# Optimization experiments

Measured on AMD Instinct MI355X. Metric: run time of the kernel, lower is better.

## Reference

```python
import jax, jax.numpy as jnp
import numpy as np

B, T, C = 1, 2048, 1024
H, HKV, DH, WIN = 16, 4, 64, 128
EPS = 1e-5


def rotate_half(x):
    x1, x2 = jnp.split(x, 2, axis=-1)
    return jnp.concatenate((-x2, x1), axis=-1)


def setup_inputs() -> dict:
    key = jax.random.key(0)
    ks = jax.random.split(key, 8)
    s = 0.02
    return {
        "x": jax.random.normal(ks[0], (B, T, C), dtype=jnp.float32),
        "Wq": jax.random.normal(ks[1], (C, H * DH), dtype=jnp.float32) * s,
        "Wk": jax.random.normal(ks[2], (C, HKV * DH), dtype=jnp.float32) * s,
        "Wv": jax.random.normal(ks[3], (C, HKV * DH), dtype=jnp.float32) * s,
        "Wc": jax.random.normal(ks[4], (C, C), dtype=jnp.float32) * s,
        "Wg": jax.random.normal(ks[5], (C, H), dtype=jnp.float32) * s,
        "bg": jax.random.normal(ks[6], (H,), dtype=jnp.float32) * s,
        "rms_w": jnp.ones((C,), dtype=jnp.float32),
    }


def reference(x, Wq, Wk, Wv, Wc, Wg, bg, rms_w):
    n_rep = H // HKV
    # projections -> [B, heads, T, DH]
    q = (x @ Wq).reshape(B, T, H, DH).transpose(0, 2, 1, 3)
    k = (x @ Wk).reshape(B, T, HKV, DH).transpose(0, 2, 1, 3)
    v = (x @ Wv).reshape(B, T, HKV, DH).transpose(0, 2, 1, 3)
    # rotary embedding (freqs duplicated across the two halves)
    inv_freq = 1.0 / (10000.0 ** (jnp.arange(0, DH, 2, dtype=jnp.float32) / DH))
    freqs = jnp.arange(T, dtype=jnp.float32)[:, None] * inv_freq[None, :]
    emb = jnp.concatenate((freqs, freqs), axis=-1)  # [T, DH]
    cos, sin = jnp.cos(emb)[None, None], jnp.sin(emb)[None, None]
    q = q * cos + rotate_half(q) * sin
    k = k * cos + rotate_half(k) * sin
    # GQA: repeat kv heads (contiguous repeat matches torch expand+reshape)
    k = jnp.repeat(k, n_rep, axis=1)
    v = jnp.repeat(v, n_rep, axis=1)
    # gated decay
    gate_logits = (x @ Wg + bg).reshape(B, T, H, 1).transpose(0, 2, 1, 3)  # [B,H,T,1]
    log_alpha = jax.nn.log_sigmoid(gate_logits)
    log_in_scale = jax.nn.log_sigmoid(-gate_logits)
    k_scaled = k * jnp.exp(log_in_scale)
    la_cum = jnp.cumsum(log_alpha, axis=2)                  # [B,H,T,1]
    log_decay = la_cum - jnp.swapaxes(la_cum, 2, 3)         # [B,H,T,T]
    causal = jnp.triu(jnp.ones((T, T), dtype=bool), k=1)
    decay = jnp.exp(jnp.where(causal, -jnp.inf, log_decay))
    scores = jnp.einsum('bhtd,bhsd->bhts', q, k_scaled)
    y_global = jnp.einsum('bhts,bhsd->bhtd', scores * decay, v)
    nb = T // WIN
    qb = q.reshape(B, H, nb, WIN, DH)
    kb = k.reshape(B, H, nb, WIN, DH)
    vb = v.reshape(B, H, nb, WIN, DH)
    att = jnp.einsum('bhnqd,bhnkd->bhnqk', qb, kb) / jnp.sqrt(jnp.float32(DH))
    wmask = jnp.triu(jnp.ones((WIN, WIN), dtype=bool), k=1)
    att = jax.nn.softmax(jnp.where(wmask, -jnp.inf, att), axis=-1)
    y_local = jnp.einsum('bhnqk,bhnkd->bhnqd', att, vb).reshape(B, H, T, DH)
    # fuse, RMSNorm, output projection
    y = (y_global + y_local).transpose(0, 2, 1, 3).reshape(B, T, C)
    y = y * jax.lax.rsqrt(jnp.mean(y * y, axis=-1, keepdims=True) + EPS) * rms_w
    return y @ Wc
```

## Files before the change

### kernel.cpp

```cpp
#include <hip/hip_runtime.h>
#include <hip/hip_bf16.h>


typedef __attribute__((ext_vector_type(8))) short bf16x8;
typedef __attribute__((ext_vector_type(4))) float f32x4;

#define MFMA16(a, b, c) __builtin_amdgcn_mfma_f32_16x16x32_bf16(a, b, c, 0, 0, 0)
#define LN10000_OVER_32 0.28782313662425575f

__device__ __forceinline__ short f2b(float f) {
  __hip_bfloat16 h = __float2bfloat16(f);
  return *reinterpret_cast<short*>(&h);
}
__device__ __forceinline__ float b2f(short s) {
  return __uint_as_float(((unsigned)(unsigned short)s) << 16);
}
__device__ __forceinline__ void gload16(const void* g, void* l) {
  __builtin_amdgcn_global_load_lds(
      (const __attribute__((address_space(1))) void*)g,
      (__attribute__((address_space(3))) void*)l, 16, 0, 0);
}

__device__ __forceinline__ void transpose_cvt64(
    const float* __restrict__ src, short* __restrict__ dst, int R, int C,
    int bx, int by, float* ts , const float* __restrict__ sw) {
  int c0 = bx * 64, r0 = by * 64;
  int tr = threadIdx.x >> 4, tc4 = (threadIdx.x & 15) * 4;
#pragma unroll
  for (int p = 0; p < 4; ++p) {
    int row = p * 16 + tr;
    float4 v = *(const float4*)&src[(size_t)(r0 + row) * C + c0 + tc4];
    ts[row * 65 + tc4] = v.x;
    ts[row * 65 + tc4 + 1] = v.y;
    ts[row * 65 + tc4 + 2] = v.z;
    ts[row * 65 + tc4 + 3] = v.w;
  }
  __syncthreads();
#pragma unroll
  for (int p = 0; p < 4; ++p) {
    int cr = p * 16 + tr;
    alignas(8) short o[4];
#pragma unroll
    for (int i = 0; i < 4; ++i) {
      int rr = tc4 + i;
      float m = sw ? sw[r0 + rr] : 1.0f;
      o[i] = f2b(ts[rr * 65 + cr] * m);
    }
    *(uint2*)&dst[(size_t)(c0 + cr) * R + r0 + tc4] = *(uint2*)o;
  }
}

__global__ __launch_bounds__(256) void prep_fused(
    const float* __restrict__ x, const float* __restrict__ Wq,
    const float* __restrict__ Wk, const float* __restrict__ Wv,
    const float* __restrict__ Wc, const float* __restrict__ Wg,
    const float* __restrict__ bg, const float* __restrict__ rmsw,
    short* __restrict__ xb, short* __restrict__ wqkvT,
    short* __restrict__ wcT, float* __restrict__ g, float* __restrict__ rs) {
  __shared__ float sbuf[64 * 65];
  const int j = blockIdx.x;
  const int tid = threadIdx.x;
  if (j < 1024) {
    const int i = j * 2048 + tid * 8;
    float4 a = *(const float4*)(x + i);
    float4 b = *(const float4*)(x + i + 4);
    alignas(16) short o[8] = {f2b(a.x), f2b(a.y), f2b(a.z), f2b(a.w),
                              f2b(b.x), f2b(b.y), f2b(b.z), f2b(b.w)};
    *(float4*)(xb + i) = *(float4*)o;
    float* xs = sbuf;
    float* part = sbuf + 2048;
    *(float4*)(xs + tid * 8) = a;
    *(float4*)(xs + tid * 8 + 4) = b;
    __syncthreads();
    const int h = tid & 15, ch = (tid >> 4) & 7, row = tid >> 7;
    const float* xr = xs + row * 1024 + ch * 128;
    const float* wgp = Wg + (size_t)(ch * 128) * 16 + h;
    float acc = 0.f;
#pragma unroll 8
    for (int k = 0; k < 128; ++k) acc = fmaf(xr[k], wgp[k * 16], acc);
    part[row * 128 + ch * 16 + h] = acc;
    __syncthreads();
    if (tid < 32) {
      int rr = tid >> 4, hh = tid & 15;
      float s = bg[hh];
#pragma unroll
      for (int cc = 0; cc < 8; ++cc) s += part[rr * 128 + cc * 16 + hh];
      g[(j * 2 + rr) * 16 + hh] = s;
    }
  } else if (j < 1280) {
    int jj = j - 1024;
    transpose_cvt64(Wq, wqkvT, 1024, 1024, jj & 15, jj >> 4, sbuf, nullptr);
  } else if (j < 1344) {
    int jj = j - 1280;
    transpose_cvt64(Wk, wqkvT + 1024 * 1024, 1024, 256, jj & 3, jj >> 2, sbuf,
                    nullptr);
  } else if (j < 1408) {
    int jj = j - 1344;
    transpose_cvt64(Wv, wqkvT + 1280 * 1024, 1024, 256, jj & 3, jj >> 2, sbuf,
                    nullptr);
  } else if (j < 1664) {
    int jj = j - 1408;
    transpose_cvt64(Wc, wcT, 1024, 1024, jj & 15, jj >> 4, sbuf, rmsw);
  } else {
    int i4 = ((j - 1664) * 256 + tid) * 4;
    float4 z = {0.f, 0.f, 0.f, 0.f};
    *(float4*)(rs + i4) = z;
  }
}

__global__ __launch_bounds__(256) void qkv_gemm_fused(
    const short* __restrict__ A, const short* __restrict__ Bt,
    short* __restrict__ qkvb, short* __restrict__ vtb,
    short* __restrict__ ktb, const float* __restrict__ g,
    float* __restrict__ lac, float* __restrict__ insc) {
  __shared__ short As[128 * 64];
  __shared__ short Bs[64 * 64];
  __shared__ float part[256];
  const int id = blockIdx.x;
  const int tid = threadIdx.x;
  if (id >= 384) {
    const int h = id - 384;
    float vals[8];
    float local = 0.f;
#pragma unroll
    for (int i = 0; i < 8; ++i) {
      int t = tid * 8 + i;
      float gv = g[t * 16 + h];
      float la = (gv > 0.f) ? -log1pf(expf(-gv)) : (gv - log1pf(expf(gv)));
      insc[h * 2048 + t] = 1.f / (1.f + expf(gv));
      vals[i] = la;
      local += la;
    }
    part[tid] = local;
    __syncthreads();
    for (int off = 1; off < 256; off <<= 1) {
      float add = (tid >= off) ? part[tid - off] : 0.f;
      __syncthreads();
      part[tid] += add;
      __syncthreads();
    }
    float run = (tid > 0) ? part[tid - 1] : 0.f;
#pragma unroll
    for (int i = 0; i < 8; ++i) {
      run += vals[i];
      lac[h * 2048 + tid * 8 + i] = run;
    }
    return;
  }
  const int lane = tid & 63, wid = tid >> 6;
  const int l15 = lane & 15, lq = lane >> 4;
  const int jlin = id >> 3;
  const int by = (id & 7) + 8 * (jlin / 24);
  const int bx = jlin % 24;
  const int m0 = by * 128, n0 = bx * 64;
  const int K = 1024;
  const int srow = lane >> 3;
  const int sc16 = (lane & 7) ^ srow;
  f32x4 acc[2][4];
#pragma unroll
  for (int mt = 0; mt < 2; ++mt)
#pragma unroll
    for (int nt = 0; nt < 4; ++nt) acc[mt][nt] = {0.f, 0.f, 0.f, 0.f};
  for (int kt = 0; kt < K; kt += 64) {
    __syncthreads();
#pragma unroll
    for (int i = 0; i < 4; ++i) {
      int jj = wid * 4 + i;
      int row = jj * 8 + srow;
      gload16(A + (size_t)(m0 + row) * K + kt + sc16 * 8, &As[jj * 512]);
    }
#pragma unroll
    for (int i = 0; i < 2; ++i) {
      int jj = wid * 2 + i;
      int row = jj * 8 + srow;
      gload16(Bt + (size_t)(n0 + row) * K + kt + sc16 * 8, &Bs[jj * 512]);
    }
    __syncthreads();
    bf16x8 af[2][2], bfr[4][2];
#pragma unroll
    for (int ks = 0; ks < 2; ++ks) {
      int c16 = ks * 4 + lq;
#pragma unroll
      for (int mt = 0; mt < 2; ++mt) {
        int ar = wid * 32 + mt * 16 + l15;
        af[mt][ks] = *(const bf16x8*)&As[(ar * 8 + (c16 ^ (ar & 7))) * 8];
      }
#pragma unroll
      for (int nt = 0; nt < 4; ++nt) {
        int br = nt * 16 + l15;
        bfr[nt][ks] = *(const bf16x8*)&Bs[(br * 8 + (c16 ^ (br & 7))) * 8];
      }
    }
#pragma unroll
    for (int ks = 0; ks < 2; ++ks)
#pragma unroll
      for (int mt = 0; mt < 2; ++mt)
#pragma unroll
        for (int nt = 0; nt < 4; ++nt)
          acc[mt][nt] = MFMA16(af[mt][ks], bfr[nt][ks], acc[mt][nt]);
  }
  if (bx >= 20) {
#pragma unroll
    for (int mt = 0; mt < 2; ++mt) {
      int row0 = m0 + wid * 32 + mt * 16 + lq * 4;
#pragma unroll
      for (int nt = 0; nt < 4; ++nt) {
        int vcol = (n0 - 1280) + nt * 16 + l15;
        alignas(8) short o4[4];
#pragma unroll
        for (int r = 0; r < 4; ++r) o4[r] = f2b(acc[mt][nt][r]);
        *(uint2*)&vtb[(size_t)vcol * 2048 + row0] = *(uint2*)o4;
      }
    }
    return;
  }
  const bool isk = (bx >= 16);
#pragma unroll
  for (int mt = 0; mt < 2; ++mt) {
    int row0 = m0 + wid * 32 + mt * 16 + lq * 4;
#pragma unroll
    for (int nt = 0; nt < 2; ++nt) {
      int d = nt * 16 + l15;
      float ivf = __expf(-LN10000_OVER_32 * (float)d);
      alignas(8) short oa[4], ob[4];
#pragma unroll
      for (int r = 0; r < 4; ++r) {
        int row_g = row0 + r;
        float th = (float)row_g * ivf;
        float cs = cosf(th), sn = sinf(th);
        float a = acc[mt][nt][r], b = acc[mt][nt + 2][r];
        oa[r] = f2b(a * cs - b * sn);
        ob[r] = f2b(b * cs + a * sn);
        qkvb[(size_t)row_g * 1536 + n0 + d] = oa[r];
        qkvb[(size_t)row_g * 1536 + n0 + d + 32] = ob[r];
      }
      if (isk) {
        int dk = n0 - 1024 + d;
        *(uint2*)&ktb[(size_t)dk * 2048 + row0] = *(uint2*)oa;
        *(uint2*)&ktb[(size_t)(dk + 32) * 2048 + row0] = *(uint2*)ob;
      }
    }
  }
}

__global__ __launch_bounds__(256) void chunk_state(
    const short* __restrict__ vtb, const short* __restrict__ ktb,
    const float* __restrict__ lac, const float* __restrict__ insc,
    short* __restrict__ Bmat) {
  __shared__ short Ks[64 * 64], Vts[64 * 64];
  __shared__ float lacs[64], inss[64], gvals[64];
  const int tid = threadIdx.x, lane = tid & 63, wid = tid >> 6;
  const int l15 = lane & 15, lq = lane >> 4;
  const int h = blockIdx.y, kh = h >> 2, c = blockIdx.x;
  const int srow = lane >> 3;
  const int sc16 = (lane & 7) ^ srow;
#pragma unroll
  for (int i = 0; i < 2; ++i) {
    int jj = wid * 2 + i;
    int row = jj * 8 + srow;
    gload16(ktb + (size_t)(kh * 64 + row) * 2048 + c * 64 + sc16 * 8,
            &Ks[jj * 512]);
    gload16(vtb + (size_t)(kh * 64 + row) * 2048 + c * 64 + sc16 * 8,
            &Vts[jj * 512]);
  }
  if (tid < 64) {
    lacs[tid] = lac[h * 2048 + c * 64 + tid];
    inss[tid] = insc[h * 2048 + c * 64 + tid];
  }
  __syncthreads();
  if (tid < 64)
    gvals[tid] = __expf(fminf(lacs[63] - lacs[tid], 0.f)) * inss[tid];
  __syncthreads();
  const int er = wid * 16 + l15;
  bf16x8 av[2];
#pragma unroll
  for (int ks = 0; ks < 2; ++ks) {
    int c16 = ks * 4 + lq;
    bf16x8 raw = *(const bf16x8*)&Vts[(er * 8 + (c16 ^ (er & 7))) * 8];
    float4 g0 = *(const float4*)&gvals[c16 * 8];
    float4 g1 = *(const float4*)&gvals[c16 * 8 + 4];
    float gv[8] = {g0.x, g0.y, g0.z, g0.w, g1.x, g1.y, g1.z, g1.w};
    bf16x8 sc;
#pragma unroll
    for (int jx = 0; jx < 8; ++jx) sc[jx] = f2b(b2f(raw[jx]) * gv[jx]);
    av[ks] = sc;
  }
  f32x4 acc[4];
#pragma unroll
  for (int nt = 0; nt < 4; ++nt) acc[nt] = {0.f, 0.f, 0.f, 0.f};
#pragma unroll
  for (int ks = 0; ks < 2; ++ks) {
    int c16 = ks * 4 + lq;
#pragma unroll
    for (int nt = 0; nt < 4; ++nt) {
      int dr = nt * 16 + l15;
      bf16x8 bk = *(const bf16x8*)&Ks[(dr * 8 + (c16 ^ (dr & 7))) * 8];
      acc[nt] = MFMA16(av[ks], bk, acc[nt]);
    }
  }
  short* Bout = Bmat + (size_t)(h * 32 + c) * 4096;
#pragma unroll
  for (int nt = 0; nt < 4; ++nt)
#pragma unroll
    for (int r = 0; r < 4; ++r) {
      int e = wid * 16 + lq * 4 + r;
      Bout[e * 64 + nt * 16 + l15] = f2b(acc[nt][r]);
    }
}

__global__ __launch_bounds__(256) void scan_kernel(
    const short* __restrict__ Bmat, const float* __restrict__ lac,
    short* __restrict__ St) {
  const int h = blockIdx.x, sl = blockIdx.y, tid = threadIdx.x;
  __shared__ float lacE[32];
  if (tid < 32) lacE[tid] = lac[h * 2048 + tid * 64 + 63];
  __syncthreads();
  const int base = sl * 512 + tid * 2;
  float S0 = 0.f, S1 = 0.f;
  *(unsigned*)&St[(size_t)(h * 32) * 4096 + base] = 0u;
  unsigned p = *(const unsigned*)&Bmat[(size_t)(h * 32) * 4096 + base];
  for (int c = 1; c < 32; ++c) {
    unsigned n = p;
    if (c < 31)
      n = *(const unsigned*)&Bmat[(size_t)(h * 32 + c) * 4096 + base];
    float a = (c >= 2) ? __expf(fminf(lacE[c - 1] - lacE[c - 2], 0.f)) : 0.f;
    S0 = fmaf(a, S0, b2f((short)(p & 0xffffu)));
    S1 = fmaf(a, S1, b2f((short)(p >> 16)));
    unsigned pack = (unsigned)(unsigned short)f2b(S0) |
                    ((unsigned)(unsigned short)f2b(S1) << 16);
    *(unsigned*)&St[(size_t)(h * 32 + c) * 4096 + base] = pack;
    p = n;
  }
}

__global__ __launch_bounds__(256) void fused_attn(
    const short* __restrict__ qkv, const short* __restrict__ vtb,
    const short* __restrict__ St, const float* __restrict__ lac,
    const float* __restrict__ insc, short* __restrict__ ys,
    float* __restrict__ rs) {
  const int c = blockIdx.x, h = blockIdx.y;
  const int kh = h >> 2;
  const bool odd = (c & 1) != 0;
  __shared__ short Qs[64 * 64], Kd[64 * 64], Vd[64 * 64], Sts[64 * 64],
      Kp[64 * 64], Vp[64 * 64], Pd[64 * 64], Pp[64 * 64];
  __shared__ float lacq[64], inss[64];
  __shared__ float laprev_sh;
  const int tid = threadIdx.x, lane = tid & 63, wid = tid >> 6;
  const int l15 = lane & 15, lq = lane >> 4;
  const int srow = lane >> 3;
  const int sc16 = (lane & 7) ^ srow;
#pragma unroll
  for (int i = 0; i < 2; ++i) {
    int jj = wid * 2 + i;
    int row = jj * 8 + srow;
    gload16(qkv + (size_t)(c * 64 + row) * 1536 + h * 64 + sc16 * 8,
            &Qs[jj * 512]);
    gload16(qkv + (size_t)(c * 64 + row) * 1536 + 1024 + kh * 64 + sc16 * 8,
            &Kd[jj * 512]);
    gload16(vtb + (size_t)(kh * 64 + row) * 2048 + c * 64 + sc16 * 8,
            &Vd[jj * 512]);
    gload16(St + (size_t)(h * 32 + c) * 4096 + row * 64 + sc16 * 8,
            &Sts[jj * 512]);
  }
  if (odd) {
#pragma unroll
    for (int i = 0; i < 2; ++i) {
      int jj = wid * 2 + i;
      int row = jj * 8 + srow;
      gload16(qkv + (size_t)((c - 1) * 64 + row) * 1536 + 1024 + kh * 64 +
                  sc16 * 8,
              &Kp[jj * 512]);
      gload16(vtb + (size_t)(kh * 64 + row) * 2048 + (c - 1) * 64 + sc16 * 8,
              &Vp[jj * 512]);
    }
  }
  if (tid < 64) {
    lacq[tid] = lac[h * 2048 + c * 64 + tid];
    inss[tid] = insc[h * 2048 + c * 64 + tid];
  }
  if (tid == 0) laprev_sh = (c > 0) ? lac[h * 2048 + c * 64 - 1] : 1e30f;
  __syncthreads();
  const int qr = wid * 16 + l15;
  bf16x8 aq[2];
#pragma unroll
  for (int ks = 0; ks < 2; ++ks) {
    int c16 = ks * 4 + lq;
    aq[ks] = *(const bf16x8*)&Qs[(qr * 8 + (c16 ^ (qr & 7))) * 8];
  }
  f32x4 sv[4];
#pragma unroll
  for (int nt = 0; nt < 4; ++nt) {
    int kr = nt * 16 + l15;
    bf16x8 bk0 = *(const bf16x8*)&Kd[(kr * 8 + ((0 + lq) ^ (kr & 7))) * 8];
    bf16x8 bk1 = *(const bf16x8*)&Kd[(kr * 8 + ((4 + lq) ^ (kr & 7))) * 8];
    f32x4 z = {0.f, 0.f, 0.f, 0.f};
    z = MFMA16(aq[0], bk0, z);
    z = MFMA16(aq[1], bk1, z);
    sv[nt] = z;
  }
  f32x4 sp[4];
  if (odd) {
#pragma unroll
    for (int nt = 0; nt < 4; ++nt) {
      int kr = nt * 16 + l15;
      bf16x8 bk0 = *(const bf16x8*)&Kp[(kr * 8 + ((0 + lq) ^ (kr & 7))) * 8];
      bf16x8 bk1 = *(const bf16x8*)&Kp[(kr * 8 + ((4 + lq) ^ (kr & 7))) * 8];
      f32x4 z = {0.f, 0.f, 0.f, 0.f};
      z = MFMA16(aq[0], bk0, z);
      z = MFMA16(aq[1], bk1, z);
      sp[nt] = z;
    }
  } else {
#pragma unroll
    for (int nt = 0; nt < 4; ++nt) sp[nt] = {0.f, 0.f, 0.f, 0.f};
  }
  f32x4 oi[4];
#pragma unroll
  for (int nt = 0; nt < 4; ++nt) {
    int er = nt * 16 + l15;
    bf16x8 bs0 = *(const bf16x8*)&Sts[(er * 8 + ((0 + lq) ^ (er & 7))) * 8];
    bf16x8 bs1 = *(const bf16x8*)&Sts[(er * 8 + ((4 + lq) ^ (er & 7))) * 8];
    f32x4 z = {0.f, 0.f, 0.f, 0.f};
    z = MFMA16(aq[0], bs0, z);
    z = MFMA16(aq[1], bs1, z);
    oi[nt] = z;
  }
  float mrow[4], ssum[4];
  float vd[4][4], vp[4][4];
#pragma unroll
  for (int r = 0; r < 4; ++r) mrow[r] = -1e30f;
#pragma unroll
  for (int nt = 0; nt < 4; ++nt) {
    int col = nt * 16 + l15;
#pragma unroll
    for (int r = 0; r < 4; ++r) {
      int row = wid * 16 + lq * 4 + r;
      float xv = (col <= row) ? sv[nt][r] * 0.125f : -1e30f;
      vd[nt][r] = xv;
      mrow[r] = fmaxf(mrow[r], xv);
      if (odd) {
        float xp = sp[nt][r] * 0.125f;
        vp[nt][r] = xp;
        mrow[r] = fmaxf(mrow[r], xp);
      }
    }
  }
#pragma unroll
  for (int r = 0; r < 4; ++r) {
    for (int off = 1; off < 16; off <<= 1)
      mrow[r] = fmaxf(mrow[r], __shfl_xor(mrow[r], off, 64));
    ssum[r] = 0.f;
  }
#pragma unroll
  for (int nt = 0; nt < 4; ++nt) {
#pragma unroll
    for (int r = 0; r < 4; ++r) {
      float e = __expf(vd[nt][r] - mrow[r]);
      vd[nt][r] = e;
      ssum[r] += e;
      if (odd) {
        float ep = __expf(vp[nt][r] - mrow[r]);
        vp[nt][r] = ep;
        ssum[r] += ep;
      }
    }
  }
#pragma unroll
  for (int r = 0; r < 4; ++r) {
    for (int off = 1; off < 16; off <<= 1) ssum[r] += __shfl_xor(ssum[r], off, 64);
    ssum[r] = 1.f / ssum[r];
  }
#pragma unroll
  for (int nt = 0; nt < 4; ++nt) {
    int col = nt * 16 + l15;
    float ls = lacq[col], is = inss[col];
#pragma unroll
    for (int r = 0; r < 4; ++r) {
      int row = wid * 16 + lq * 4 + r;
      float w = __expf(fminf(lacq[row] - ls, 0.f)) * is;
      if (col > row) w = 0.f;
      float pc = sv[nt][r] * w + vd[nt][r] * ssum[r];
      Pd[(row * 8 + ((col >> 3) ^ (row & 7))) * 8 + (col & 7)] = f2b(pc);
      if (odd)
        Pp[(row * 8 + ((col >> 3) ^ (row & 7))) * 8 + (col & 7)] =
            f2b(vp[nt][r] * ssum[r]);
    }
  }
  __syncthreads();
  bf16x8 ap[2];
#pragma unroll
  for (int ks = 0; ks < 2; ++ks) {
    int c16 = ks * 4 + lq;
    ap[ks] = *(const bf16x8*)&Pd[(qr * 8 + (c16 ^ (qr & 7))) * 8];
  }
  f32x4 o[4];
#pragma unroll
  for (int nt = 0; nt < 4; ++nt) {
    int vr = nt * 16 + l15;
    bf16x8 bv0 = *(const bf16x8*)&Vd[(vr * 8 + ((0 + lq) ^ (vr & 7))) * 8];
    bf16x8 bv1 = *(const bf16x8*)&Vd[(vr * 8 + ((4 + lq) ^ (vr & 7))) * 8];
    f32x4 z = {0.f, 0.f, 0.f, 0.f};
    z = MFMA16(ap[0], bv0, z);
    z = MFMA16(ap[1], bv1, z);
    o[nt] = z;
  }
  if (odd) {
    bf16x8 app[2];
#pragma unroll
    for (int ks = 0; ks < 2; ++ks) {
      int c16 = ks * 4 + lq;
      app[ks] = *(const bf16x8*)&Pp[(qr * 8 + (c16 ^ (qr & 7))) * 8];
    }
#pragma unroll
    for (int nt = 0; nt < 4; ++nt) {
      int vr = nt * 16 + l15;
      bf16x8 bv0 = *(const bf16x8*)&Vp[(vr * 8 + ((0 + lq) ^ (vr & 7))) * 8];
      bf16x8 bv1 = *(const bf16x8*)&Vp[(vr * 8 + ((4 + lq) ^ (vr & 7))) * 8];
      o[nt] = MFMA16(app[0], bv0, o[nt]);
      o[nt] = MFMA16(app[1], bv1, o[nt]);
    }
  }
  const float laprev = laprev_sh;
#pragma unroll
  for (int r = 0; r < 4; ++r) {
    int row = wid * 16 + lq * 4 + r;
    float rfac = __expf(fminf(lacq[row] - laprev, 0.f));
    int row_g = c * 64 + row;
    float ssq = 0.f;
#pragma unroll
    for (int nt = 0; nt < 4; ++nt) {
      int colg = h * 64 + nt * 16 + l15;
      size_t idx = (size_t)row_g * 1024 + colg;
      float v = o[nt][r] + rfac * oi[nt][r];
      ys[idx] = f2b(v);
      ssq = fmaf(v, v, ssq);
    }
    for (int off = 1; off < 16; off <<= 1) ssq += __shfl_xor(ssq, off, 64);
    if (l15 == 0) atomicAdd(&rs[row_g], ssq);
  }
}

__global__ __launch_bounds__(256) void out_gemm(
    const short* __restrict__ A, const short* __restrict__ Bt,
    const float* __restrict__ rs, float* __restrict__ C) {
  __shared__ short As[64 * 64];
  __shared__ short Bs[64 * 64];
  const int tid = threadIdx.x, lane = tid & 63, wid = tid >> 6;
  const int l15 = lane & 15, lq = lane >> 4;
  const int wm = wid >> 1, wn = wid & 1;
  const int id = blockIdx.x;
  const int jlin = id >> 3;
  const int by = (id & 7) + 8 * (jlin / 16);
  const int bx = jlin % 16;
  const int m0 = by * 64, n0 = bx * 64;
  const int K = 1024;
  const int srow = lane >> 3;
  const int sc16 = (lane & 7) ^ srow;
  f32x4 acc[2][2];
#pragma unroll
  for (int mt = 0; mt < 2; ++mt)
#pragma unroll
    for (int nt = 0; nt < 2; ++nt) acc[mt][nt] = {0.f, 0.f, 0.f, 0.f};
  for (int kt = 0; kt < K; kt += 64) {
    __syncthreads();
#pragma unroll
    for (int i = 0; i < 2; ++i) {
      int jj = wid * 2 + i;
      int row = jj * 8 + srow;
      gload16(A + (size_t)(m0 + row) * K + kt + sc16 * 8, &As[jj * 512]);
      gload16(Bt + (size_t)(n0 + row) * K + kt + sc16 * 8, &Bs[jj * 512]);
    }
    __syncthreads();
    bf16x8 af[2][2], bfr[2][2];
#pragma unroll
    for (int ks = 0; ks < 2; ++ks) {
      int c16 = ks * 4 + lq;
#pragma unroll
      for (int mt = 0; mt < 2; ++mt) {
        int ar = wm * 32 + mt * 16 + l15;
        af[mt][ks] = *(const bf16x8*)&As[(ar * 8 + (c16 ^ (ar & 7))) * 8];
      }
#pragma unroll
      for (int nt = 0; nt < 2; ++nt) {
        int br = wn * 32 + nt * 16 + l15;
        bfr[nt][ks] = *(const bf16x8*)&Bs[(br * 8 + (c16 ^ (br & 7))) * 8];
      }
    }
#pragma unroll
    for (int ks = 0; ks < 2; ++ks)
#pragma unroll
      for (int mt = 0; mt < 2; ++mt)
#pragma unroll
        for (int nt = 0; nt < 2; ++nt)
          acc[mt][nt] = MFMA16(af[mt][ks], bfr[nt][ks], acc[mt][nt]);
  }
#pragma unroll
  for (int mt = 0; mt < 2; ++mt) {
    int row0 = m0 + wm * 32 + mt * 16 + lq * 4;
#pragma unroll
    for (int r = 0; r < 4; ++r) {
      int row_g = row0 + r;
      float sc = rsqrtf(rs[row_g] * (1.0f / 1024.0f) + 1e-5f);
#pragma unroll
      for (int nt = 0; nt < 2; ++nt)
        C[(size_t)row_g * 1024 + n0 + wn * 32 + nt * 16 + l15] =
            acc[mt][nt][r] * sc;
    }
  }
}

extern "C" void kernel_launch(void* const* d_in, const int* in_sizes, int n_in,
                              void* d_out, int out_size, void* d_ws,
                              size_t ws_size, hipStream_t stream) {
  const float* x = (const float*)d_in[0];
  const float* Wq = (const float*)d_in[1];
  const float* Wk = (const float*)d_in[2];
  const float* Wv = (const float*)d_in[3];
  const float* Wc = (const float*)d_in[4];
  const float* Wg = (const float*)d_in[5];
  const float* bg = (const float*)d_in[6];
  const float* rmsw = (const float*)d_in[7];
  float* out = (float*)d_out;

  short* wqkvT = (short*)d_ws;
  short* wcT = wqkvT + 1536 * 1024;
  short* qkvb = wcT + 1024 * 1024;
  short* vtb = qkvb + 2048 * 1536;
  short* ktb = vtb + 256 * 2048;
  float* gw = (float*)(ktb + 256 * 2048);
  float* lacw = gw + 2048 * 16;
  float* inscw = lacw + 16 * 2048;
  short* Bmat = (short*)(inscw + 16 * 2048);
  short* Stb = Bmat + 16 * 32 * 4096;
  short* xb = Stb + 16 * 32 * 4096;
  short* ys = xb;
  float* rsq = (float*)(xb + 2048 * 1024);

  prep_fused<<<1666, 256, 0, stream>>>(x, Wq, Wk, Wv, Wc, Wg, bg, rmsw, xb,
                                       wqkvT, wcT, gw, rsq);
  qkv_gemm_fused<<<400, 256, 0, stream>>>(xb, wqkvT, qkvb, vtb, ktb, gw, lacw,
                                          inscw);
  chunk_state<<<dim3(32, 16), 256, 0, stream>>>(vtb, ktb, lacw, inscw, Bmat);
  scan_kernel<<<dim3(16, 8), 256, 0, stream>>>(Bmat, lacw, Stb);
  fused_attn<<<dim3(32, 16), 256, 0, stream>>>(qkvb, vtb, Stb, lacw, inscw,
                                               ys, rsq);
  out_gemm<<<512, 256, 0, stream>>>(ys, wcT, rsq, out);
}
```

Before: 129.9 us.

## Move Wc transpose and rs zeroing into QKV GEMM launch; preload scan inputs

```diff
diff --git a/kernel.cpp b/kernel.cpp
--- a/kernel.cpp
+++ b/kernel.cpp
@@ -53,10 +53,9 @@
 __global__ __launch_bounds__(256) void prep_fused(
     const float* __restrict__ x, const float* __restrict__ Wq,
     const float* __restrict__ Wk, const float* __restrict__ Wv,
-    const float* __restrict__ Wc, const float* __restrict__ Wg,
-    const float* __restrict__ bg, const float* __restrict__ rmsw,
+    const float* __restrict__ Wg, const float* __restrict__ bg,
     short* __restrict__ xb, short* __restrict__ wqkvT,
-    short* __restrict__ wcT, float* __restrict__ g, float* __restrict__ rs) {
+    float* __restrict__ g) {
   __shared__ float sbuf[64 * 65];
   const int j = blockIdx.x;
   const int tid = threadIdx.x;
@@ -94,17 +93,10 @@
     int jj = j - 1280;
     transpose_cvt64(Wk, wqkvT + 1024 * 1024, 1024, 256, jj & 3, jj >> 2, sbuf,
                     nullptr);
-  } else if (j < 1408) {
+  } else {
     int jj = j - 1344;
     transpose_cvt64(Wv, wqkvT + 1280 * 1024, 1024, 256, jj & 3, jj >> 2, sbuf,
                     nullptr);
-  } else if (j < 1664) {
-    int jj = j - 1408;
-    transpose_cvt64(Wc, wcT, 1024, 1024, jj & 15, jj >> 4, sbuf, rmsw);
-  } else {
-    int i4 = ((j - 1664) * 256 + tid) * 4;
-    float4 z = {0.f, 0.f, 0.f, 0.f};
-    *(float4*)(rs + i4) = z;
   }
 }
 
@@ -112,12 +104,27 @@
     const short* __restrict__ A, const short* __restrict__ Bt,
     short* __restrict__ qkvb, short* __restrict__ vtb,
     short* __restrict__ ktb, const float* __restrict__ g,
-    float* __restrict__ lac, float* __restrict__ insc) {
-  __shared__ short As[128 * 64];
-  __shared__ short Bs[64 * 64];
-  __shared__ float part[256];
+    float* __restrict__ lac, float* __restrict__ insc,
+    const float* __restrict__ Wc, const float* __restrict__ rmsw,
+    short* __restrict__ wcT, float* __restrict__ rs) {
+  __shared__ __align__(16) short smem[128 * 64 + 64 * 64 + 512];
+  short* As = smem;
+  short* Bs = smem + 128 * 64;
+  float* part = (float*)(smem + 128 * 64 + 64 * 64);
+  float* ts = (float*)smem;
   const int id = blockIdx.x;
   const int tid = threadIdx.x;
+  if (id >= 400) {
+    if (id < 656) {
+      int jj = id - 400;
+      transpose_cvt64(Wc, wcT, 1024, 1024, jj & 15, jj >> 4, ts, rmsw);
+    } else {
+      int i4 = ((id - 656) * 256 + tid) * 4;
+      float4 z = {0.f, 0.f, 0.f, 0.f};
+      *(float4*)(rs + i4) = z;
+    }
+    return;
+  }
   if (id >= 384) {
     const int h = id - 384;
     float vals[8];
@@ -314,22 +321,23 @@
   const int h = blockIdx.x, sl = blockIdx.y, tid = threadIdx.x;
   __shared__ float lacE[32];
   if (tid < 32) lacE[tid] = lac[h * 2048 + tid * 64 + 63];
+  const int base = sl * 512 + tid * 2;
+  unsigned pv[31];
+#pragma unroll
+  for (int c = 0; c < 31; ++c)
+    pv[c] = *(const unsigned*)&Bmat[(size_t)(h * 32 + c) * 4096 + base];
   __syncthreads();
-  const int base = sl * 512 + tid * 2;
   float S0 = 0.f, S1 = 0.f;
   *(unsigned*)&St[(size_t)(h * 32) * 4096 + base] = 0u;
-  unsigned p = *(const unsigned*)&Bmat[(size_t)(h * 32) * 4096 + base];
+#pragma unroll
   for (int c = 1; c < 32; ++c) {
-    unsigned n = p;
-    if (c < 31)
-      n = *(const unsigned*)&Bmat[(size_t)(h * 32 + c) * 4096 + base];
     float a = (c >= 2) ? __expf(fminf(lacE[c - 1] - lacE[c - 2], 0.f)) : 0.f;
+    unsigned p = pv[c - 1];
     S0 = fmaf(a, S0, b2f((short)(p & 0xffffu)));
     S1 = fmaf(a, S1, b2f((short)(p >> 16)));
     unsigned pack = (unsigned)(unsigned short)f2b(S0) |
                     ((unsigned)(unsigned short)f2b(S1) << 16);
     *(unsigned*)&St[(size_t)(h * 32 + c) * 4096 + base] = pack;
-    p = n;
   }
 }
 
@@ -636,10 +644,9 @@
   short* ys = xb;
   float* rsq = (float*)(xb + 2048 * 1024);
 
-  prep_fused<<<1666, 256, 0, stream>>>(x, Wq, Wk, Wv, Wc, Wg, bg, rmsw, xb,
-                                       wqkvT, wcT, gw, rsq);
-  qkv_gemm_fused<<<400, 256, 0, stream>>>(xb, wqkvT, qkvb, vtb, ktb, gw, lacw,
-                                          inscw);
+  prep_fused<<<1408, 256, 0, stream>>>(x, Wq, Wk, Wv, Wg, bg, xb, wqkvT, gw);
+  qkv_gemm_fused<<<658, 256, 0, stream>>>(xb, wqkvT, qkvb, vtb, ktb, gw, lacw,
+                                          inscw, Wc, rmsw, wcT, rsq);
   chunk_state<<<dim3(32, 16), 256, 0, stream>>>(vtb, ktb, lacw, inscw, Bmat);
   scan_kernel<<<dim3(16, 8), 256, 0, stream>>>(Bmat, lacw, Stb);
   fused_attn<<<dim3(32, 16), 256, 0, stream>>>(qkvb, vtb, Stb, lacw, inscw,
```

Measured after the change: 129.0 us (median of 3 runs). About the same (-0.7%).
